# Performance work log

Measured on AMD Instinct MI355X. Metric: run time of the kernel, lower is better.

The kernel has to match this reference:

```python
import jax, jax.numpy as jnp
import numpy as np

B, D, L = 4, 64, 4096  # batch, pos feature dim (=pos_learnable_dim), sequence length

def setup_inputs() -> dict:
    key = jax.random.key(0)
    k1, k2 = jax.random.split(key, 2)
    pos_embed = jax.random.normal(k1, (B, D, L), dtype=jnp.float32)
    # _LinearWithBias(D, D): torch weight [out, in], bias [out]
    W_pos = (jax.random.normal(k2, (D, D), dtype=jnp.float32) / np.float32(np.sqrt(D)))
    b_pos = jnp.zeros((D,), dtype=jnp.float32)
    SOFTPLUS0 = 0.6931472  # softplus(0) = ln 2, gpytorch default raw param -> constrained value
    lengthscale = jnp.asarray(SOFTPLUS0, dtype=jnp.float32)   # RBFKernel lengthscale
    outputscale = jnp.asarray(SOFTPLUS0, dtype=jnp.float32)   # ScaleKernel outputscale
    return {"pos_embed": pos_embed, "W_pos": W_pos, "b_pos": b_pos,
            "lengthscale": lengthscale, "outputscale": outputscale}

def reference(pos_embed, W_pos, b_pos, lengthscale, outputscale):
    # pos_embed: [B, D, L]
    x = jnp.swapaxes(pos_embed, 1, 2)          # [B, L, D] (transpose, linear, transpose back, transpose again)
    x = x @ W_pos.T + b_pos                    # learnable positional linear on feature dim
    # gpytorch ScaleKernel(RBFKernel): outputscale * exp(-0.5 * ||(x_i - x_j)/lengthscale||^2)
    xs = x / lengthscale                       # [B, L, D]
    sq = jnp.sum(xs * xs, axis=-1)             # [B, L]
    sq_dist = sq[:, :, None] + sq[:, None, :] - 2.0 * jnp.einsum('bld,bmd->blm', xs, xs)
    sq_dist = jnp.maximum(sq_dist, 0.0)        # gpytorch clamps sq dist at 0
    return outputscale * jnp.exp(-0.5 * sq_dist)  # [B, L, L]
```

## Files before the change

kernel.cpp:

```cpp
#include <hip/hip_runtime.h>

using bf16x8 = __attribute__((ext_vector_type(8))) __bf16;
using f32x16 = __attribute__((ext_vector_type(16))) float;

#define BB 4
#define DD 64
#define LL 4096

__global__ __launch_bounds__(256) void prep_kernel(
    const float* __restrict__ pe,
    const float* __restrict__ W,
    const float* __restrict__ bias,
    const float* __restrict__ ls,
    __bf16* __restrict__ xs,
    float* __restrict__ h)
{
    __shared__ float pe_lds[DD][64];
    __shared__ float W_lds[DD * DD];
    __shared__ float hpart[4][64];

    const int tid = threadIdx.x;
    const int blk = blockIdx.x;
    const int b  = blk >> 6;
    const int l0 = (blk & 63) * 64;

    {
        const int l = tid & 63;
        const int kb = tid >> 6;
        #pragma unroll
        for (int it = 0; it < 16; ++it) {
            const int k = it * 4 + kb;
            pe_lds[k][l] = pe[((size_t)b * DD + k) * LL + l0 + l];
        }
    }
    #pragma unroll
    for (int it = 0; it < 16; ++it)
        W_lds[it * 256 + tid] = W[it * 256 + tid];
    __syncthreads();

    const int w = tid >> 6;
    const int l = tid & 63;
    const float SQRT_LOG2E = 1.2011224087864498f;
    const float scale = SQRT_LOG2E / ls[0];

    float acc[16];
    #pragma unroll
    for (int i = 0; i < 16; ++i) acc[i] = bias[w * 16 + i];

    for (int k4 = 0; k4 < 16; ++k4) {
        const float p0 = pe_lds[k4 * 4 + 0][l];
        const float p1 = pe_lds[k4 * 4 + 1][l];
        const float p2 = pe_lds[k4 * 4 + 2][l];
        const float p3 = pe_lds[k4 * 4 + 3][l];
        #pragma unroll
        for (int i = 0; i < 16; ++i) {
            const float4 wv = *(const float4*)&W_lds[(w * 16 + i) * DD + k4 * 4];
            acc[i] += p0 * wv.x + p1 * wv.y + p2 * wv.z + p3 * wv.w;
        }
    }

    unsigned short out16[16];
    float hs = 0.0f;
    #pragma unroll
    for (int i = 0; i < 16; ++i) {
        const float xf = acc[i] * scale;
        const __bf16 bv = (__bf16)xf;
        const float xr = (float)bv;
        hs += xr * xr;
        out16[i] = __builtin_bit_cast(unsigned short, bv);
    }
    {
        __bf16* dst = xs + ((size_t)b * LL + l0 + l) * DD + w * 16;
        *(uint4*)dst       = *(const uint4*)&out16[0];
        *(uint4*)(dst + 8) = *(const uint4*)&out16[8];
    }
    hpart[w][l] = hs;
    __syncthreads();
    if (tid < 64) {
        const float s = hpart[0][tid] + hpart[1][tid] + hpart[2][tid] + hpart[3][tid];
        h[(size_t)b * LL + tid + l0] = 0.5f * s;
    }
}

__global__ __launch_bounds__(256, 4) void gram_kernel(
    const __bf16* __restrict__ xs,
    const float* __restrict__ h,
    const float* __restrict__ osc,
    float* __restrict__ out)
{
    const int bid = blockIdx.x;
    const int b  = bid >> 11;
    const int t  = bid & 2047;
    const int ti = t >> 6;
    const int tj = t & 63;

    const int tid  = threadIdx.x;
    const int wid  = tid >> 6;
    const int lane = tid & 63;
    const int lr = lane & 31, lg = lane >> 5;

    const int rows0 = ti * 128 + wid * 32;
    const int cols0 = tj * 64;

    const __bf16* xsb = xs + (size_t)b * LL * DD;
    const float*  hb  = h + (size_t)b * LL;

    bf16x8 af[4], bg[2][4];
    #pragma unroll
    for (int kk = 0; kk < 4; ++kk)
        af[kk] = *(const bf16x8*)(xsb + (size_t)(rows0 + lr) * DD + kk * 16 + lg * 8);
    #pragma unroll
    for (int nt = 0; nt < 2; ++nt)
        #pragma unroll
        for (int kk = 0; kk < 4; ++kk)
            bg[nt][kk] = *(const bf16x8*)(xsb + (size_t)(cols0 + nt * 32 + lr) * DD + kk * 16 + lg * 8);

    f32x16 acc[2];
    acc[0] = (f32x16)(0.0f);
    acc[1] = (f32x16)(0.0f);

    #pragma unroll
    for (int kk = 0; kk < 4; ++kk) {
        acc[0] = __builtin_amdgcn_mfma_f32_32x32x16_bf16(af[kk], bg[0][kk], acc[0], 0, 0, 0);
        acc[1] = __builtin_amdgcn_mfma_f32_32x32x16_bf16(af[kk], bg[1][kk], acc[1], 0, 0, 0);
    }

    const float c = osc[0];

    float hi[16];
    #pragma unroll
    for (int r = 0; r < 16; ++r)
        hi[r] = hb[rows0 + (r & 3) + 8 * (r >> 2) + 4 * lg];

    #pragma unroll
    for (int nt = 0; nt < 2; ++nt) {
        const int col = cols0 + nt * 32 + lr;
        const float hj = hb[col];
        #pragma unroll
        for (int r = 0; r < 16; ++r) {
            const int row = rows0 + (r & 3) + 8 * (r >> 2) + 4 * lg;
            float tt = acc[nt][r] - hi[r] - hj;
            tt = fminf(tt, 0.0f);
            const float v = c * __builtin_amdgcn_exp2f(tt);
            __builtin_nontemporal_store(v, &out[((size_t)b * LL + row) * LL + col]);
        }
    }
}

extern "C" void kernel_launch(void* const* d_in, const int* in_sizes, int n_in,
                              void* d_out, int out_size, void* d_ws, size_t ws_size,
                              hipStream_t stream) {
    const float* pe   = (const float*)d_in[0];
    const float* W    = (const float*)d_in[1];
    const float* bias = (const float*)d_in[2];
    const float* ls   = (const float*)d_in[3];
    const float* osc  = (const float*)d_in[4];
    float* out = (float*)d_out;

    __bf16* xs = (__bf16*)d_ws;
    float*  h  = (float*)((char*)d_ws + (size_t)BB * LL * DD * 2);

    prep_kernel<<<256, 256, 0, stream>>>(pe, W, bias, ls, xs, h);
    gram_kernel<<<BB * 32 * 64, 256, 0, stream>>>(xs, h, osc, out);
}
```

Measured before the change: 73.02 us.

## Enlarge gram tile to 128x128 per block and fold outputscale into exponent

```diff
diff --git a/kernel.cpp b/kernel.cpp
--- a/kernel.cpp
+++ b/kernel.cpp
@@ -89,60 +89,62 @@
     float* __restrict__ out)
 {
     const int bid = blockIdx.x;
-    const int b  = bid >> 11;
-    const int t  = bid & 2047;
-    const int ti = t >> 6;
-    const int tj = t & 63;
+    const int b  = bid >> 10;
+    const int t  = bid & 1023;
+    const int ti = t >> 5, tj = t & 31;
 
     const int tid  = threadIdx.x;
     const int wid  = tid >> 6;
     const int lane = tid & 63;
     const int lr = lane & 31, lg = lane >> 5;
 
-    const int rows0 = ti * 128 + wid * 32;
-    const int cols0 = tj * 64;
+    const int rows0 = ti * 128 + (wid >> 1) * 64;
+    const int cols0 = tj * 128 + (wid & 1) * 64;
 
     const __bf16* xsb = xs + (size_t)b * LL * DD;
     const float*  hb  = h + (size_t)b * LL;
 
-    bf16x8 af[4], bg[2][4];
-    #pragma unroll
-    for (int kk = 0; kk < 4; ++kk)
-        af[kk] = *(const bf16x8*)(xsb + (size_t)(rows0 + lr) * DD + kk * 16 + lg * 8);
-    #pragma unroll
-    for (int nt = 0; nt < 2; ++nt)
+    const float c  = osc[0];
+    const float lc = __builtin_log2f(c);
+
+    #pragma unroll 1
+    for (int mt = 0; mt < 2; ++mt) {
+        const int r0 = rows0 + mt * 32;
+
+        bf16x8 af[4];
         #pragma unroll
         for (int kk = 0; kk < 4; ++kk)
-            bg[nt][kk] = *(const bf16x8*)(xsb + (size_t)(cols0 + nt * 32 + lr) * DD + kk * 16 + lg * 8);
+            af[kk] = *(const bf16x8*)(xsb + (size_t)(r0 + lr) * DD + kk * 16 + lg * 8);
 
-    f32x16 acc[2];
-    acc[0] = (f32x16)(0.0f);
-    acc[1] = (f32x16)(0.0f);
+        float hi2[16];
+        #pragma unroll
+        for (int r = 0; r < 16; ++r)
+            hi2[r] = hb[r0 + (r & 3) + 8 * (r >> 2) + 4 * lg] - lc;
 
-    #pragma unroll
-    for (int kk = 0; kk < 4; ++kk) {
-        acc[0] = __builtin_amdgcn_mfma_f32_32x32x16_bf16(af[kk], bg[0][kk], acc[0], 0, 0, 0);
-        acc[1] = __builtin_amdgcn_mfma_f32_32x32x16_bf16(af[kk], bg[1][kk], acc[1], 0, 0, 0);
-    }
+        #pragma unroll 1
+        for (int nt = 0; nt < 2; ++nt) {
+            const int c0 = cols0 + nt * 32;
 
-    const float c = osc[0];
+            bf16x8 bg[4];
+            #pragma unroll
+            for (int kk = 0; kk < 4; ++kk)
+                bg[kk] = *(const bf16x8*)(xsb + (size_t)(c0 + lr) * DD + kk * 16 + lg * 8);
 
-    float hi[16];
-    #pragma unroll
-    for (int r = 0; r < 16; ++r)
-        hi[r] = hb[rows0 + (r & 3) + 8 * (r >> 2) + 4 * lg];
+            f32x16 acc = (f32x16)(0.0f);
+            #pragma unroll
+            for (int kk = 0; kk < 4; ++kk)
+                acc = __builtin_amdgcn_mfma_f32_32x32x16_bf16(af[kk], bg[kk], acc, 0, 0, 0);
 
-    #pragma unroll
-    for (int nt = 0; nt < 2; ++nt) {
-        const int col = cols0 + nt * 32 + lr;
-        const float hj = hb[col];
-        #pragma unroll
-        for (int r = 0; r < 16; ++r) {
-            const int row = rows0 + (r & 3) + 8 * (r >> 2) + 4 * lg;
-            float tt = acc[nt][r] - hi[r] - hj;
-            tt = fminf(tt, 0.0f);
-            const float v = c * __builtin_amdgcn_exp2f(tt);
-            __builtin_nontemporal_store(v, &out[((size_t)b * LL + row) * LL + col]);
+            const int col = c0 + lr;
+            const float hj = hb[col];
+            float* op = out + ((size_t)b * LL + r0 + 4 * lg) * LL + col;
+            #pragma unroll
+            for (int r = 0; r < 16; ++r) {
+                float tt = acc[r] - hi2[r] - hj;
+                tt = fminf(tt, lc);
+                const int rowoff = (r & 3) + 8 * (r >> 2);
+                op[(size_t)rowoff * LL] = __builtin_amdgcn_exp2f(tt);
+            }
         }
     }
 }
@@ -161,5 +163,5 @@
     float*  h  = (float*)((char*)d_ws + (size_t)BB * LL * DD * 2);
 
     prep_kernel<<<256, 256, 0, stream>>>(pe, W, bias, ls, xs, h);
-    gram_kernel<<<BB * 32 * 64, 256, 0, stream>>>(xs, h, osc, out);
+    gram_kernel<<<BB * 32 * 32, 256, 0, stream>>>(xs, h, osc, out);
 }
```

New measurement: 75.03 us. +2.7%, slower.
